# Kernel optimization log

Measured on AMD Instinct MI355X. Metric: run time of the kernel, lower is better.

The kernel has to match this reference:

```python
import jax, jax.numpy as jnp
import numpy as np

ALPHA = 0.2   # LeakyReLU negative slope
OF = 64       # out_features


def setup_inputs() -> dict:
    key = jax.random.key(0)
    k1, k2, k3, k4 = jax.random.split(key, 4)
    h = jax.random.normal(k1, (16, 2048, 12, 128), dtype=jnp.float32)
    adj = jax.random.randint(k2, (2, 6, 6), 0, 2, dtype=jnp.int32)
    # learned params (xavier-like scale)
    W = jax.random.normal(k3, (128, 64), dtype=jnp.float32) * 0.1
    a = jax.random.normal(k4, (2, 2 * OF, 1), dtype=jnp.float32) * 0.1
    return {"h": h, "adj": adj, "W": W, "a": a}


def reference(h, adj, W, a):
    # h: [B, N, 12, Fin], adj: [2, 6, 6], W: [Fin, OF], a: [2, 2*OF, 1]
    Wh = jnp.einsum('bnkf,fo->bnko', h, W)  # [B, N, 12, OF]
    outs = []
    for i in range(2):  # fixed 2 chunks of 6 nodes (h.shape[2] // 6)
        chunk = Wh[:, :, i * 6:(i + 1) * 6, :]       # [B, N, 6, OF]
        # matmul(a_input, a[i]) decomposes: e_pq = a1.Wh_p + a2.Wh_q
        a1 = a[i, :OF, 0]
        a2 = a[i, OF:, 0]
        s1 = chunk @ a1                               # [B, N, 6]
        s2 = chunk @ a2                               # [B, N, 6]
        e = jax.nn.leaky_relu(s1[..., :, None] + s2[..., None, :], ALPHA)  # [B,N,6,6]
        ei = e[i]                                     # NOTE: batch index i, as in source
        att = jnp.where(adj[i] > 0, ei, jnp.float32(-9e15))  # [N, 6, 6]
        att = jax.nn.softmax(att, axis=-1)
        # dropout omitted (eval mode)
        outs.append(jnp.einsum('npq,bnqf->bnpf', att, chunk))  # [B, N, 6, OF]
    h_prime = jnp.concatenate(outs, axis=2)           # [B, N, 12, OF]
    return jax.nn.elu(h_prime)                        # concat=True -> ELU
```

## Files before the change

### kernel.cpp

```cpp
#include <hip/hip_runtime.h>
#include <math.h>

#define LRELU_ALPHA 0.2f
#define NEG_BIG -9000000000000000.0f

#define WA_OFF 147456
#define WF_OFF 147968

typedef __attribute__((ext_vector_type(8))) short bf16x8;
typedef __attribute__((ext_vector_type(4))) float f32x4;

static __device__ inline unsigned short f2bf(float x) {
    unsigned int u = __float_as_uint(x);
    unsigned int r = (u + 0x7FFFu + ((u >> 16) & 1u)) >> 16;
    return (unsigned short)r;
}

__global__ __launch_bounds__(256) void gat_prep_kernel(
    const float* __restrict__ W, const float* __restrict__ a,
    float* __restrict__ ws)
{
    const int tid = threadIdx.x;
    if (blockIdx.x < 32) {
        short* wf = (short*)(ws + WF_OFF);
        const int o = blockIdx.x * 256 + tid;
        const int n = o >> 7, k = o & 127;
        wf[o] = (short)f2bf(W[k * 64 + n]);
    } else {
        float* wa = ws + WA_OFF;
        for (int idx = tid; idx < 512; idx += 256) {
            const int gi = idx >> 8, j = (idx >> 7) & 1, c = idx & 127;
            const float* Wr = W + c * 64;
            const float* ar = a + gi * 128 + j * 64;
            float s = 0.f;
#pragma unroll
            for (int f = 0; f < 64; ++f) s = fmaf(Wr[f], ar[f], s);
            wa[idx] = s;
        }
    }
}

__global__ __launch_bounds__(256) void gat_att_kernel(
    const float* __restrict__ h, const int* __restrict__ adj,
    float* __restrict__ ws)
{
    const int warp = threadIdx.x >> 6;
    const int lane = threadIdx.x & 63;
    const int iw = blockIdx.x * 4 + warp;
    const int gi = iw >> 11;
    const int n  = iw & 2047;

    const float* wa = ws + WA_OFF;
    const float2 w1 = *(const float2*)(wa + gi * 256 + 2 * lane);
    const float2 w2 = *(const float2*)(wa + gi * 256 + 128 + 2 * lane);
    const float* hp = h + ((size_t)(gi * 2048 + n) * 12 + (size_t)gi * 6) * 128 + 2 * lane;

    float t1[6], t2[6];
#pragma unroll
    for (int q = 0; q < 6; ++q) {
        const float2 hq = *(const float2*)(hp + q * 128);
        t1[q] = hq.x * w1.x + hq.y * w1.y;
        t2[q] = hq.x * w2.x + hq.y * w2.y;
    }
#pragma unroll
    for (int off = 32; off > 0; off >>= 1) {
#pragma unroll
        for (int q = 0; q < 6; ++q) {
            t1[q] += __shfl_xor(t1[q], off, 64);
            t2[q] += __shfl_xor(t2[q], off, 64);
        }
    }

    if (lane < 6) {
        const int p = lane;
        float s1p = t1[0];
#pragma unroll
        for (int q = 1; q < 6; ++q) { if (p == q) s1p = t1[q]; }

        float row[6];
        float mx = -3.0e38f;
#pragma unroll
        for (int q = 0; q < 6; ++q) {
            float e = s1p + t2[q];
            e = (e > 0.f) ? e : (LRELU_ALPHA * e);
            const int ad = adj[gi * 36 + p * 6 + q];
            const float m = (ad > 0) ? e : NEG_BIG;
            row[q] = m;
            mx = fmaxf(mx, m);
        }
        float sum = 0.f;
#pragma unroll
        for (int q = 0; q < 6; ++q) {
            row[q] = expf(row[q] - mx);
            sum += row[q];
        }
        const float inv = 1.f / sum;
        float* op = ws + (size_t)iw * 36 + p * 6;
#pragma unroll
        for (int q = 0; q < 6; ++q) op[q] = row[q] * inv;
    }
}

#define PSTR 136
__global__ __launch_bounds__(256) void gat_main_mfma(
    const float* __restrict__ h, const float* __restrict__ ws,
    float* __restrict__ out)
{
    __shared__ __align__(16) short lds[4 * 48 * PSTR];
    const int tid  = threadIdx.x;
    const int warp = tid >> 6;
    const int lane = tid & 63;
    short* Pw = lds + warp * 48 * PSTR;

    const int wave_id = blockIdx.x * 4 + warp;
    const int bn0 = wave_id * 4;
    const int half = lane >> 5;
    const int li   = lane & 31;

    for (int pair = 0; pair < 2; ++pair) {
        const int bno = pair * 2 + half;
        const int bn  = bn0 + bno;
        const int n   = bn & 2047;

        const float* hb = h + (size_t)bn * 1536 + li * 4;
        float4 hv[12];
#pragma unroll
        for (int r = 0; r < 12; ++r)
            hv[r] = *(const float4*)(hb + r * 128);

#pragma unroll
        for (int gi = 0; gi < 2; ++gi) {
            const float4* ap = (const float4*)(ws + (size_t)(gi * 2048 + n) * 36);
            float attv[36];
#pragma unroll
            for (int j = 0; j < 9; ++j) {
                const float4 av = ap[j];
                attv[j * 4 + 0] = av.x; attv[j * 4 + 1] = av.y;
                attv[j * 4 + 2] = av.z; attv[j * 4 + 3] = av.w;
            }
#pragma unroll
            for (int p = 0; p < 6; ++p) {
                float ax = 0.f, ay = 0.f, az = 0.f, aw = 0.f;
#pragma unroll
                for (int q = 0; q < 6; ++q) {
                    const float apq = attv[p * 6 + q];
                    const float4 hq = hv[gi * 6 + q];
                    ax = fmaf(apq, hq.x, ax);
                    ay = fmaf(apq, hq.y, ay);
                    az = fmaf(apq, hq.z, az);
                    aw = fmaf(apq, hq.w, aw);
                }
                const int row = bno * 12 + gi * 6 + p;
                ushort4 pk;
                pk.x = f2bf(ax); pk.y = f2bf(ay);
                pk.z = f2bf(az); pk.w = f2bf(aw);
                *(ushort4*)(Pw + row * PSTR + li * 4) = pk;
            }
        }
    }

    const short* wf = (const short*)(ws + WF_OFF);
    const int col  = lane & 15;
    const int quad = lane >> 4;
    f32x4 acc[3][4];
#pragma unroll
    for (int mt = 0; mt < 3; ++mt)
#pragma unroll
        for (int nt = 0; nt < 4; ++nt)
            acc[mt][nt] = (f32x4){0.f, 0.f, 0.f, 0.f};

#pragma unroll
    for (int ks = 0; ks < 4; ++ks) {
        bf16x8 bfr[4];
#pragma unroll
        for (int nt = 0; nt < 4; ++nt)
            bfr[nt] = *(const bf16x8*)(wf + (nt * 16 + col) * 128 + ks * 32 + quad * 8);
        bf16x8 afr[3];
#pragma unroll
        for (int mt = 0; mt < 3; ++mt)
            afr[mt] = *(const bf16x8*)(Pw + (mt * 16 + col) * PSTR + ks * 32 + quad * 8);
#pragma unroll
        for (int mt = 0; mt < 3; ++mt)
#pragma unroll
            for (int nt = 0; nt < 4; ++nt)
                acc[mt][nt] = __builtin_amdgcn_mfma_f32_16x16x32_bf16(
                    afr[mt], bfr[nt], acc[mt][nt], 0, 0, 0);
    }

    float* ob = out + (size_t)bn0 * 768;
#pragma unroll
    for (int mt = 0; mt < 3; ++mt)
#pragma unroll
        for (int nt = 0; nt < 4; ++nt)
#pragma unroll
            for (int r = 0; r < 4; ++r) {
                const int row = mt * 16 + quad * 4 + r;
                float v = acc[mt][nt][r];
                v = (v > 0.f) ? v : (expf(v) - 1.f);
                ob[row * 64 + nt * 16 + col] = v;
            }
}

extern "C" void kernel_launch(void* const* d_in, const int* in_sizes, int n_in,
                              void* d_out, int out_size, void* d_ws, size_t ws_size,
                              hipStream_t stream) {
    const float* h   = (const float*)d_in[0];
    const int*   adj = (const int*)d_in[1];
    const float* W   = (const float*)d_in[2];
    const float* a   = (const float*)d_in[3];
    float* out = (float*)d_out;
    float* ws  = (float*)d_ws;

    hipLaunchKernelGGL(gat_prep_kernel, dim3(33), dim3(256), 0, stream, W, a, ws);
    hipLaunchKernelGGL(gat_att_kernel, dim3(1024), dim3(256), 0, stream, h, adj, ws);
    hipLaunchKernelGGL(gat_main_mfma, dim3(2048), dim3(256), 0, stream, h, ws, out);
}
```

Measured before the change: 331.4 us.

## Fuse attention softmax into the MFMA main kernel with per-node block mapping

Removes the separate attention kernel. Each block now handles one node index across all 16 batches, and warp 0 computes the two 6x6 softmax matrices from the h rows it already loaded (batches 0 and 1). The matrices go into shared memory, which avoids the workspace round trip, the extra h reads and one kernel launch. The cost is a block-wide barrier while one wave computes attention, plus batch-strided output and input addressing instead of contiguous per-wave chunks.

```diff
diff --git a/kernel.cpp b/kernel.cpp
--- a/kernel.cpp
+++ b/kernel.cpp
@@ -4,8 +4,8 @@
 #define LRELU_ALPHA 0.2f
 #define NEG_BIG -9000000000000000.0f
 
-#define WA_OFF 147456
-#define WF_OFF 147968
+#define WA_OFF 0
+#define WF_OFF 512
 
 typedef __attribute__((ext_vector_type(8))) short bf16x8;
 typedef __attribute__((ext_vector_type(4))) float f32x4;
@@ -24,8 +24,8 @@
     if (blockIdx.x < 32) {
         short* wf = (short*)(ws + WF_OFF);
         const int o = blockIdx.x * 256 + tid;
-        const int n = o >> 7, k = o & 127;
-        wf[o] = (short)f2bf(W[k * 64 + n]);
+        const int nn = o >> 7, k = o & 127;
+        wf[o] = (short)f2bf(W[k * 64 + nn]);
     } else {
         float* wa = ws + WA_OFF;
         for (int idx = tid; idx < 512; idx += 256) {
@@ -40,101 +40,90 @@
     }
 }
 
-__global__ __launch_bounds__(256) void gat_att_kernel(
+#define PSTR 136
+__global__ __launch_bounds__(256) void gat_fused(
     const float* __restrict__ h, const int* __restrict__ adj,
-    float* __restrict__ ws)
-{
-    const int warp = threadIdx.x >> 6;
-    const int lane = threadIdx.x & 63;
-    const int iw = blockIdx.x * 4 + warp;
-    const int gi = iw >> 11;
-    const int n  = iw & 2047;
-
-    const float* wa = ws + WA_OFF;
-    const float2 w1 = *(const float2*)(wa + gi * 256 + 2 * lane);
-    const float2 w2 = *(const float2*)(wa + gi * 256 + 128 + 2 * lane);
-    const float* hp = h + ((size_t)(gi * 2048 + n) * 12 + (size_t)gi * 6) * 128 + 2 * lane;
-
-    float t1[6], t2[6];
-#pragma unroll
-    for (int q = 0; q < 6; ++q) {
-        const float2 hq = *(const float2*)(hp + q * 128);
-        t1[q] = hq.x * w1.x + hq.y * w1.y;
-        t2[q] = hq.x * w2.x + hq.y * w2.y;
-    }
-#pragma unroll
-    for (int off = 32; off > 0; off >>= 1) {
-#pragma unroll
-        for (int q = 0; q < 6; ++q) {
-            t1[q] += __shfl_xor(t1[q], off, 64);
-            t2[q] += __shfl_xor(t2[q], off, 64);
-        }
-    }
-
-    if (lane < 6) {
-        const int p = lane;
-        float s1p = t1[0];
-#pragma unroll
-        for (int q = 1; q < 6; ++q) { if (p == q) s1p = t1[q]; }
-
-        float row[6];
-        float mx = -3.0e38f;
-#pragma unroll
-        for (int q = 0; q < 6; ++q) {
-            float e = s1p + t2[q];
-            e = (e > 0.f) ? e : (LRELU_ALPHA * e);
-            const int ad = adj[gi * 36 + p * 6 + q];
-            const float m = (ad > 0) ? e : NEG_BIG;
-            row[q] = m;
-            mx = fmaxf(mx, m);
-        }
-        float sum = 0.f;
-#pragma unroll
-        for (int q = 0; q < 6; ++q) {
-            row[q] = expf(row[q] - mx);
-            sum += row[q];
-        }
-        const float inv = 1.f / sum;
-        float* op = ws + (size_t)iw * 36 + p * 6;
-#pragma unroll
-        for (int q = 0; q < 6; ++q) op[q] = row[q] * inv;
-    }
-}
-
-#define PSTR 136
-__global__ __launch_bounds__(256) void gat_main_mfma(
-    const float* __restrict__ h, const float* __restrict__ ws,
-    float* __restrict__ out)
+    const float* __restrict__ ws, float* __restrict__ out)
 {
     __shared__ __align__(16) short lds[4 * 48 * PSTR];
+    __shared__ float att_lds[2][36];
+
     const int tid  = threadIdx.x;
     const int warp = tid >> 6;
     const int lane = tid & 63;
-    short* Pw = lds + warp * 48 * PSTR;
-
-    const int wave_id = blockIdx.x * 4 + warp;
-    const int bn0 = wave_id * 4;
     const int half = lane >> 5;
     const int li   = lane & 31;
+    const int n    = blockIdx.x;
+    short* Pw = lds + warp * 48 * PSTR;
+
+    const float* hb0 = h + (size_t)((warp * 4 + half) * 2048 + n) * 1536 + li * 4;
+    float4 hv[12];
+#pragma unroll
+    for (int r = 0; r < 12; ++r)
+        hv[r] = *(const float4*)(hb0 + r * 128);
+
+    if (warp == 0) {
+        const int gi = half;
+        const float4 w1a = *(const float4*)(ws + WA_OFF + gi * 256 + li * 4);
+        const float4 w2a = *(const float4*)(ws + WA_OFF + gi * 256 + 128 + li * 4);
+        float t1[6], t2[6];
+#pragma unroll
+        for (int q = 0; q < 6; ++q) {
+            const float4 hq = hv[gi * 6 + q];
+            t1[q] = hq.x * w1a.x + hq.y * w1a.y + hq.z * w1a.z + hq.w * w1a.w;
+            t2[q] = hq.x * w2a.x + hq.y * w2a.y + hq.z * w2a.z + hq.w * w2a.w;
+        }
+#pragma unroll
+        for (int off = 16; off > 0; off >>= 1) {
+#pragma unroll
+            for (int q = 0; q < 6; ++q) {
+                t1[q] += __shfl_xor(t1[q], off, 64);
+                t2[q] += __shfl_xor(t2[q], off, 64);
+            }
+        }
+        if (li < 6) {
+            const int p = li;
+            float s1p = t1[0];
+#pragma unroll
+            for (int q = 1; q < 6; ++q) { if (p == q) s1p = t1[q]; }
+            float row[6];
+            float mx = -3.0e38f;
+#pragma unroll
+            for (int q = 0; q < 6; ++q) {
+                float e = s1p + t2[q];
+                e = (e > 0.f) ? e : (LRELU_ALPHA * e);
+                const int ad = adj[gi * 36 + p * 6 + q];
+                const float m = (ad > 0) ? e : NEG_BIG;
+                row[q] = m;
+                mx = fmaxf(mx, m);
+            }
+            float sum = 0.f;
+#pragma unroll
+            for (int q = 0; q < 6; ++q) {
+                row[q] = expf(row[q] - mx);
+                sum += row[q];
+            }
+            const float inv = 1.f / sum;
+#pragma unroll
+            for (int q = 0; q < 6; ++q) att_lds[gi][p * 6 + q] = row[q] * inv;
+        }
+    }
+    __syncthreads();
 
     for (int pair = 0; pair < 2; ++pair) {
         const int bno = pair * 2 + half;
-        const int bn  = bn0 + bno;
-        const int n   = bn & 2047;
-
-        const float* hb = h + (size_t)bn * 1536 + li * 4;
-        float4 hv[12];
-#pragma unroll
-        for (int r = 0; r < 12; ++r)
-            hv[r] = *(const float4*)(hb + r * 128);
-
+        if (pair == 1) {
+            const float* hb = h + (size_t)((warp * 4 + bno) * 2048 + n) * 1536 + li * 4;
+#pragma unroll
+            for (int r = 0; r < 12; ++r)
+                hv[r] = *(const float4*)(hb + r * 128);
+        }
 #pragma unroll
         for (int gi = 0; gi < 2; ++gi) {
-            const float4* ap = (const float4*)(ws + (size_t)(gi * 2048 + n) * 36);
             float attv[36];
 #pragma unroll
             for (int j = 0; j < 9; ++j) {
-                const float4 av = ap[j];
+                const float4 av = *(const float4*)(&att_lds[gi][j * 4]);
                 attv[j * 4 + 0] = av.x; attv[j * 4 + 1] = av.y;
                 attv[j * 4 + 2] = av.z; attv[j * 4 + 3] = av.w;
             }
@@ -187,7 +176,7 @@
                     afr[mt], bfr[nt], acc[mt][nt], 0, 0, 0);
     }
 
-    float* ob = out + (size_t)bn0 * 768;
+    float* ob = out + (size_t)(warp * 4) * 1572864 + (size_t)n * 768;
 #pragma unroll
     for (int mt = 0; mt < 3; ++mt)
 #pragma unroll
@@ -195,9 +184,11 @@
 #pragma unroll
             for (int r = 0; r < 4; ++r) {
                 const int row = mt * 16 + quad * 4 + r;
+                const int bl = row / 12;
+                const int kl = row - bl * 12;
                 float v = acc[mt][nt][r];
                 v = (v > 0.f) ? v : (expf(v) - 1.f);
-                ob[row * 64 + nt * 16 + col] = v;
+                ob[(size_t)bl * 1572864 + kl * 64 + nt * 16 + col] = v;
             }
 }
 
@@ -212,6 +203,5 @@
     float* ws  = (float*)d_ws;
 
     hipLaunchKernelGGL(gat_prep_kernel, dim3(33), dim3(256), 0, stream, W, a, ws);
-    hipLaunchKernelGGL(gat_att_kernel, dim3(1024), dim3(256), 0, stream, h, adj, ws);
-    hipLaunchKernelGGL(gat_main_mfma, dim3(2048), dim3(256), 0, stream, h, ws, out);
-}
+    hipLaunchKernelGGL(gat_fused, dim3(2048), dim3(256), 0, stream, h, adj, ws, out);
+}
```

Result: slower. 392.8 us (+18.5%).

## Split main kernel work across warps per block with shared P tile

Applied to the files above, without the earlier changes.

Restructures the main kernel so each block handles 4 (b,n) rows, one per warp. Each half-warp covers one 6-node group, and the four warps then split the 64 output columns of the MFMA product over a shared 48-row P tile in LDS. Attention weights are staged once per block in LDS, and h loads and output stores use nontemporal hints. The grid grows from 2048 to 8192 blocks with fewer registers per thread and an occupancy hint, aiming at more latency hiding for this memory-bound kernel. The cost is extra block barriers and smaller per-block work.

```diff
diff --git a/kernel.cpp b/kernel.cpp
--- a/kernel.cpp
+++ b/kernel.cpp
@@ -102,103 +102,88 @@
 }
 
 #define PSTR 136
-__global__ __launch_bounds__(256) void gat_main_mfma(
+__global__ __launch_bounds__(256, 8) void gat_main_mfma(
     const float* __restrict__ h, const float* __restrict__ ws,
     float* __restrict__ out)
 {
-    __shared__ __align__(16) short lds[4 * 48 * PSTR];
+    __shared__ __align__(16) short Pl[48 * PSTR];
+    __shared__ __align__(16) float attl[288];
+
     const int tid  = threadIdx.x;
     const int warp = tid >> 6;
     const int lane = tid & 63;
-    short* Pw = lds + warp * 48 * PSTR;
-
-    const int wave_id = blockIdx.x * 4 + warp;
-    const int bn0 = wave_id * 4;
     const int half = lane >> 5;
     const int li   = lane & 31;
-
-    for (int pair = 0; pair < 2; ++pair) {
-        const int bno = pair * 2 + half;
-        const int bn  = bn0 + bno;
-        const int n   = bn & 2047;
-
-        const float* hb = h + (size_t)bn * 1536 + li * 4;
-        float4 hv[12];
-#pragma unroll
-        for (int r = 0; r < 12; ++r)
-            hv[r] = *(const float4*)(hb + r * 128);
-
-#pragma unroll
-        for (int gi = 0; gi < 2; ++gi) {
-            const float4* ap = (const float4*)(ws + (size_t)(gi * 2048 + n) * 36);
-            float attv[36];
-#pragma unroll
-            for (int j = 0; j < 9; ++j) {
-                const float4 av = ap[j];
-                attv[j * 4 + 0] = av.x; attv[j * 4 + 1] = av.y;
-                attv[j * 4 + 2] = av.z; attv[j * 4 + 3] = av.w;
-            }
-#pragma unroll
-            for (int p = 0; p < 6; ++p) {
-                float ax = 0.f, ay = 0.f, az = 0.f, aw = 0.f;
-#pragma unroll
-                for (int q = 0; q < 6; ++q) {
-                    const float apq = attv[p * 6 + q];
-                    const float4 hq = hv[gi * 6 + q];
-                    ax = fmaf(apq, hq.x, ax);
-                    ay = fmaf(apq, hq.y, ay);
-                    az = fmaf(apq, hq.z, az);
-                    aw = fmaf(apq, hq.w, aw);
-                }
-                const int row = bno * 12 + gi * 6 + p;
-                ushort4 pk;
-                pk.x = f2bf(ax); pk.y = f2bf(ay);
-                pk.z = f2bf(az); pk.w = f2bf(aw);
-                *(ushort4*)(Pw + row * PSTR + li * 4) = pk;
-            }
-        }
-    }
+    const int bn0  = blockIdx.x * 4;
+    const int n0   = bn0 & 2047;
+
+    for (int i = tid; i < 288; i += 256) {
+        const int gi = i / 144;
+        const int rem = i - gi * 144;
+        const int nn = rem / 36;
+        const int e  = rem - nn * 36;
+        attl[i] = ws[(size_t)(gi * 2048 + n0 + nn) * 36 + e];
+    }
+
+    const int bn = bn0 + warp;
+    const int gi = half;
+    const float* hb = h + (size_t)bn * 1536 + gi * 6 * 128 + li * 4;
+    f32x4 hv[6];
+#pragma unroll
+    for (int r = 0; r < 6; ++r)
+        hv[r] = __builtin_nontemporal_load((const f32x4*)(hb + r * 128));
+
+    __syncthreads();
+
+    const float* av = attl + gi * 144 + warp * 36;
+#pragma unroll
+    for (int p = 0; p < 6; ++p) {
+        float ax = 0.f, ay = 0.f, az = 0.f, aw = 0.f;
+#pragma unroll
+        for (int q = 0; q < 6; ++q) {
+            const float apq = av[p * 6 + q];
+            const f32x4 hq = hv[q];
+            ax = fmaf(apq, hq[0], ax);
+            ay = fmaf(apq, hq[1], ay);
+            az = fmaf(apq, hq[2], az);
+            aw = fmaf(apq, hq[3], aw);
+        }
+        const int row = warp * 12 + gi * 6 + p;
+        ushort4 pk;
+        pk.x = f2bf(ax); pk.y = f2bf(ay);
+        pk.z = f2bf(az); pk.w = f2bf(aw);
+        *(ushort4*)(Pl + row * PSTR + li * 4) = pk;
+    }
+
+    __syncthreads();
 
     const short* wf = (const short*)(ws + WF_OFF);
     const int col  = lane & 15;
     const int quad = lane >> 4;
-    f32x4 acc[3][4];
+    f32x4 acc[3];
+#pragma unroll
+    for (int mt = 0; mt < 3; ++mt) acc[mt] = (f32x4){0.f, 0.f, 0.f, 0.f};
+
+#pragma unroll
+    for (int ks = 0; ks < 4; ++ks) {
+        const bf16x8 bfr = *(const bf16x8*)(wf + (warp * 16 + col) * 128 + ks * 32 + quad * 8);
+#pragma unroll
+        for (int mt = 0; mt < 3; ++mt) {
+            const bf16x8 afr = *(const bf16x8*)(Pl + (mt * 16 + col) * PSTR + ks * 32 + quad * 8);
+            acc[mt] = __builtin_amdgcn_mfma_f32_16x16x32_bf16(afr, bfr, acc[mt], 0, 0, 0);
+        }
+    }
+
+    float* ob = out + (size_t)bn0 * 768 + warp * 16 + col;
 #pragma unroll
     for (int mt = 0; mt < 3; ++mt)
 #pragma unroll
-        for (int nt = 0; nt < 4; ++nt)
-            acc[mt][nt] = (f32x4){0.f, 0.f, 0.f, 0.f};
-
-#pragma unroll
-    for (int ks = 0; ks < 4; ++ks) {
-        bf16x8 bfr[4];
-#pragma unroll
-        for (int nt = 0; nt < 4; ++nt)
-            bfr[nt] = *(const bf16x8*)(wf + (nt * 16 + col) * 128 + ks * 32 + quad * 8);
-        bf16x8 afr[3];
-#pragma unroll
-        for (int mt = 0; mt < 3; ++mt)
-            afr[mt] = *(const bf16x8*)(Pw + (mt * 16 + col) * PSTR + ks * 32 + quad * 8);
-#pragma unroll
-        for (int mt = 0; mt < 3; ++mt)
-#pragma unroll
-            for (int nt = 0; nt < 4; ++nt)
-                acc[mt][nt] = __builtin_amdgcn_mfma_f32_16x16x32_bf16(
-                    afr[mt], bfr[nt], acc[mt][nt], 0, 0, 0);
-    }
-
-    float* ob = out + (size_t)bn0 * 768;
-#pragma unroll
-    for (int mt = 0; mt < 3; ++mt)
-#pragma unroll
-        for (int nt = 0; nt < 4; ++nt)
-#pragma unroll
-            for (int r = 0; r < 4; ++r) {
-                const int row = mt * 16 + quad * 4 + r;
-                float v = acc[mt][nt][r];
-                v = (v > 0.f) ? v : (expf(v) - 1.f);
-                ob[row * 64 + nt * 16 + col] = v;
-            }
+        for (int r = 0; r < 4; ++r) {
+            const int row = mt * 16 + quad * 4 + r;
+            float v = acc[mt][r];
+            v = (v > 0.f) ? v : (expf(v) - 1.f);
+            __builtin_nontemporal_store(v, ob + row * 64);
+        }
 }
 
 extern "C" void kernel_launch(void* const* d_in, const int* in_sizes, int n_in,
@@ -213,5 +198,5 @@
 
     hipLaunchKernelGGL(gat_prep_kernel, dim3(33), dim3(256), 0, stream, W, a, ws);
     hipLaunchKernelGGL(gat_att_kernel, dim3(1024), dim3(256), 0, stream, h, adj, ws);
-    hipLaunchKernelGGL(gat_main_mfma, dim3(2048), dim3(256), 0, stream, h, ws, out);
-}
+    hipLaunchKernelGGL(gat_main_mfma, dim3(8192), dim3(256), 0, stream, h, ws, out);
+}
```

Measured after the change: 316.2 us. -4.6%, faster.
